# Kernel tuning notes

Measured on AMD Instinct MI355X. Metric: run time of the kernel, lower is better.

Reference implementation:

```python
import jax, jax.numpy as jnp
import numpy as np

B, T, E, L = 512, 20, 256, 2          # batch, path_length, embedding_size, LSTM layers
VE, VA = 50000, 1000                  # entity / action vocab
M = 4                                 # use_entity_embeddings -> m=4
D = M * E                             # LSTMCell input size  (1024)
H = M * 256                           # LSTMCell hidden size (m*hidden_size = 1024)


def setup_inputs() -> dict:
    key = jax.random.key(0)
    ks = jax.random.split(key, 14)
    s = 1.0 / np.sqrt(H)
    ent_emb = (jax.random.normal(ks[0], (VE, 2 * E), jnp.float32) * 0.02).at[0].set(0.0)
    rel_emb = (jax.random.normal(ks[1], (VA, 2 * E), jnp.float32) * 0.02).at[0].set(0.0)
    inp = {
        "entity_batch": jax.random.randint(ks[2], (B, T), 1, VE, jnp.int32),
        "relation_batch": jax.random.randint(ks[3], (B, T), 1, VA, jnp.int32),
        "query_relations": jax.random.randint(ks[4], (B,), 1, VA, jnp.int32),
        "data_length": jax.random.randint(ks[5], (B,), 1, T + 1, jnp.int32),
        "ent_emb": ent_emb,
        "rel_emb": rel_emb,
        "W_ih": jax.random.uniform(ks[6], (L, 4 * H, D), jnp.float32, -s, s),
        "W_hh": jax.random.uniform(ks[7], (L, 4 * H, H), jnp.float32, -s, s),
        "b_ih": jax.random.uniform(ks[8], (L, 4 * H), jnp.float32, -s, s),
        "b_hh": jax.random.uniform(ks[9], (L, 4 * H), jnp.float32, -s, s),
        "W1": jax.random.uniform(ks[10], (4 * 256, H), jnp.float32, -s, s),   # Linear(m*hidden, 4*hidden)
        "b1": jax.random.uniform(ks[11], (4 * 256,), jnp.float32, -s, s),
        "W2": jax.random.uniform(ks[12], (2, 4 * 256), jnp.float32, -0.05, 0.05),
        "b2": jax.random.uniform(ks[13], (2,), jnp.float32, -0.05, 0.05),
    }
    return inp


def reference(entity_batch, relation_batch, query_relations, data_length,
              ent_emb, rel_emb, W_ih, W_hh, b_ih, b_hh, W1, b1, W2, b2):
    # action encoder: concat(relation_emb, entity_emb) -> [B, T, 4E]
    x = jnp.concatenate([rel_emb[relation_batch], ent_emb[entity_batch]], axis=-1)
    xs = jnp.swapaxes(x, 0, 1)  # [T, B, 4E]

    def step(carry, xt):
        hs, cs = carry  # each [L, B, H]
        new_h, new_c = [], []
        for i in range(L):
            # NOTE: faithful to source — every layer consumes xt (prev_action_embeddings)
            g = xt @ W_ih[i].T + b_ih[i] + hs[i] @ W_hh[i].T + b_hh[i]  # [B, 4H]
            gi, gf, gg, go = jnp.split(g, 4, axis=-1)
            c = jax.nn.sigmoid(gf) * cs[i] + jax.nn.sigmoid(gi) * jnp.tanh(gg)
            h = jax.nn.sigmoid(go) * jnp.tanh(c)
            new_h.append(h)
            new_c.append(c)
        return (jnp.stack(new_h), jnp.stack(new_c)), new_h[-1]

    init = (jnp.zeros((L, B, H), jnp.float32), jnp.zeros((L, B, H), jnp.float32))
    _, outs = jax.lax.scan(step, init, xs)       # [T, B, H]
    outs = jnp.swapaxes(outs, 0, 1)              # [B, T, H]

    # gather output at position data_length-1 per row
    idx = (data_length - 1).astype(jnp.int32)[:, None, None]
    sel = jnp.take_along_axis(outs, idx, axis=1)[:, 0, :]  # [B, H]

    # policy MLP: Linear -> ReLU -> Linear -> ReLU, then squeeze (no-op for [B,2])
    y = jax.nn.relu(sel @ W1.T + b1)
    y = jax.nn.relu(y @ W2.T + b2)
    return jnp.squeeze(y)
```

## Files before the change

### kernel.cpp

```cpp
#include <hip/hip_runtime.h>

typedef __bf16 bf16x8 __attribute__((ext_vector_type(8)));
typedef __bf16 bf16x4 __attribute__((ext_vector_type(4)));
typedef float  f32x4  __attribute__((ext_vector_type(4)));

#define MFMA16 __builtin_amdgcn_mfma_f32_16x16x32_bf16

__device__ __forceinline__ float fsig(float x)  { return 1.f / (1.f + __expf(-x)); }
__device__ __forceinline__ float ftanh(float x) { return 1.f - 2.f / (__expf(2.f * x) + 1.f); }


__global__ __launch_bounds__(512) void prep(
    const float* __restrict__ Wih, const float* __restrict__ Whh,
    const float* __restrict__ W1,  const float* __restrict__ bih,
    const float* __restrict__ bhh, const int* __restrict__ dlen,
    __bf16* __restrict__ Wih1, __bf16* __restrict__ Whh1,
    __bf16* __restrict__ W1b,  float* __restrict__ bsum,
    int* __restrict__ perm, int* __restrict__ dl_s, int* __restrict__ n_act)
{
    const int tid = threadIdx.x;
    if (blockIdx.x < 2048) {
        const size_t L1 = 4096UL * 1024UL;
        size_t i = (size_t)blockIdx.x * 512 + tid;
        float4 a = *(const float4*)(Wih + L1 + i * 4);
        float4 b = *(const float4*)(Whh + L1 + i * 4);
        bf16x4 av = { (__bf16)a.x, (__bf16)a.y, (__bf16)a.z, (__bf16)a.w };
        bf16x4 bv = { (__bf16)b.x, (__bf16)b.y, (__bf16)b.z, (__bf16)b.w };
        *(bf16x4*)(Wih1 + i * 4) = av;
        *(bf16x4*)(Whh1 + i * 4) = bv;
        W1b[i] = (__bf16)W1[i];
        if (i < 4096) bsum[i] = bih[4096 + i] + bhh[4096 + i];
    } else {
        __shared__ int sdl[512];
        const int b = tid;
        const int dl = dlen[b];
        sdl[b] = dl;
        __syncthreads();
        int pos = 0;
        for (int j = 0; j < 512; ++j) {
            const int dj = sdl[j];
            pos += (dj > dl) || (dj == dl && j < b);
        }
        perm[pos] = b;
        dl_s[pos] = dl;
        if (b < 20) {
            int cnt = 0;
            for (int j = 0; j < 512; ++j) cnt += (sdl[j] > b);
            n_act[b] = cnt;
        }
    }
}

__global__ __launch_bounds__(256) void gather_x(
    const int* __restrict__ ent, const int* __restrict__ rel,
    const float* __restrict__ ent_emb, const float* __restrict__ rel_emb,
    const int* __restrict__ perm, __bf16* __restrict__ xbf)
{
    int bid = blockIdx.x;
    int sb = bid / 20, t = bid - sb * 20;
    int bo = perm[sb];
    int tid = threadIdx.x;
    int col = (tid & 127) * 4;
    const float* src = (tid < 128)
        ? (rel_emb + (size_t)rel[bo * 20 + t] * 512 + col)
        : (ent_emb + (size_t)ent[bo * 20 + t] * 512 + col);
    float4 v = *(const float4*)src;
    bf16x4 o = { (__bf16)v.x, (__bf16)v.y, (__bf16)v.z, (__bf16)v.w };
    int outcol = (tid < 128) ? col : (512 + col);
    *(bf16x4*)(xbf + (size_t)(t * 512 + sb) * 1024 + outcol) = o;
}

template<bool RELU, bool SKIP>
__global__ __launch_bounds__(256) void gemm_bias(
    const __bf16* __restrict__ A, const __bf16* __restrict__ B,
    const float* __restrict__ bias, __bf16* __restrict__ C,
    int M, int N, int K, const int* __restrict__ nact)
{
    const int m0 = blockIdx.y * 128, n0 = blockIdx.x * 128;
    if (SKIP) {
        if ((m0 & 511) >= nact[m0 >> 9]) return;
    }
    __shared__ __bf16 As[2][128 * 64];
    __shared__ __bf16 Bs[2][128 * 64];
    const int tid = threadIdx.x;
    const int w = tid >> 6, lane = tid & 63;
    const int wr = (w >> 1) * 64, wc = (w & 1) * 64;
    const int srow = w * 32 + (lane >> 3);
    const int scol = (((lane & 7) ^ (lane >> 3)) << 3);
    const int wofs = srow * 64 + (lane & 7) * 8;

    f32x4 acc[4][4] = {};
    bf16x8 ar[4], br[4];

#pragma unroll
    for (int j = 0; j < 4; ++j) {
        ar[j] = *(const bf16x8*)(A + (size_t)(m0 + srow + j * 8) * K + scol);
        br[j] = *(const bf16x8*)(B + (size_t)(n0 + srow + j * 8) * K + scol);
    }
    for (int k0 = 0, i = 0; k0 < K; k0 += 64, ++i) {
        const int cur = i & 1;
#pragma unroll
        for (int j = 0; j < 4; ++j) {
            *(bf16x8*)&As[cur][wofs + j * 512] = ar[j];
            *(bf16x8*)&Bs[cur][wofs + j * 512] = br[j];
        }
        if (k0 + 64 < K) {
#pragma unroll
            for (int j = 0; j < 4; ++j) {
                ar[j] = *(const bf16x8*)(A + (size_t)(m0 + srow + j * 8) * K + k0 + 64 + scol);
                br[j] = *(const bf16x8*)(B + (size_t)(n0 + srow + j * 8) * K + k0 + 64 + scol);
            }
        }
        __syncthreads();
#pragma unroll
        for (int ks = 0; ks < 2; ++ks) {
            const int ko = (((ks * 4 + (lane >> 4)) ^ (lane & 7)) << 3);
            bf16x8 af[4], bb[4];
#pragma unroll
            for (int ii = 0; ii < 4; ++ii)
                af[ii] = *(const bf16x8*)&As[cur][(wr + ii * 16 + (lane & 15)) * 64 + ko];
#pragma unroll
            for (int j = 0; j < 4; ++j)
                bb[j] = *(const bf16x8*)&Bs[cur][(wc + j * 16 + (lane & 15)) * 64 + ko];
#pragma unroll
            for (int ii = 0; ii < 4; ++ii)
#pragma unroll
                for (int j = 0; j < 4; ++j)
                    acc[ii][j] = MFMA16(af[ii], bb[j], acc[ii][j], 0, 0, 0);
        }
    }
    const int rbase = m0 + wr + (lane >> 4) * 4;
    const int cbase = n0 + wc + (lane & 15);
#pragma unroll
    for (int j = 0; j < 4; ++j) {
        const int col = cbase + j * 16;
        const float bv = bias[col];
#pragma unroll
        for (int i = 0; i < 4; ++i)
#pragma unroll
            for (int r = 0; r < 4; ++r) {
                float v = acc[i][j][r] + bv;
                if (RELU) v = fmaxf(v, 0.f);
                C[(size_t)(rbase + i * 16 + r) * N + col] = (__bf16)v;
            }
    }
}

__global__ __launch_bounds__(256) void lstm_step(
    const __bf16* __restrict__ h_in, const __bf16* __restrict__ Whh,
    const __bf16* __restrict__ Xg, float* __restrict__ cst,
    __bf16* __restrict__ h_out, __bf16* __restrict__ sel,
    const int* __restrict__ dl_s, const int* __restrict__ perm,
    const int* __restrict__ n_act, int t)
{
    const int nt = n_act[t];
    const int m0 = blockIdx.y * 32;
    if (m0 >= nt) return;
    __shared__ __bf16 As[2][32 * 64];
    __shared__ __bf16 Bs[2][128 * 64];
    const int tid = threadIdx.x;
    const int w = tid >> 6, lane = tid & 63;
    const int j0 = blockIdx.x * 32;
    const int rh  = w >> 1;
    const int chq = w & 1;

    const int brow = tid >> 3;
    const int seg  = tid & 7;
    const int swc  = ((seg ^ (brow & 7)) << 3);
    const __bf16* gB = Whh + (size_t)(j0 + brow) * 1024 + swc;
    const __bf16* gA = h_in + (size_t)(m0 + brow) * 1024 + swc;

    f32x4 a0 = {0,0,0,0}, a1 = {0,0,0,0}, a2 = {0,0,0,0}, a3 = {0,0,0,0};
    bf16x8 rb0, rb1, rb2, rb3, ra;

    rb0 = *(const bf16x8*)(gB);
    rb1 = *(const bf16x8*)(gB + 1024UL * 1024);
    rb2 = *(const bf16x8*)(gB + 2048UL * 1024);
    rb3 = *(const bf16x8*)(gB + 3072UL * 1024);
    ra  = *(const bf16x8*)(gA);

    for (int k0 = 0, i = 0; k0 < 1024; k0 += 64, ++i) {
        const int cur = i & 1;
        *(bf16x8*)&Bs[cur][(0 * 32 + brow) * 64 + seg * 8] = rb0;
        *(bf16x8*)&Bs[cur][(1 * 32 + brow) * 64 + seg * 8] = rb1;
        *(bf16x8*)&Bs[cur][(2 * 32 + brow) * 64 + seg * 8] = rb2;
        *(bf16x8*)&Bs[cur][(3 * 32 + brow) * 64 + seg * 8] = rb3;
        *(bf16x8*)&As[cur][brow * 64 + seg * 8] = ra;
        if (k0 + 64 < 1024) {
            rb0 = *(const bf16x8*)(gB + k0 + 64);
            rb1 = *(const bf16x8*)(gB + 1024UL * 1024 + k0 + 64);
            rb2 = *(const bf16x8*)(gB + 2048UL * 1024 + k0 + 64);
            rb3 = *(const bf16x8*)(gB + 3072UL * 1024 + k0 + 64);
            ra  = *(const bf16x8*)(gA + k0 + 64);
        }
        __syncthreads();
#pragma unroll
        for (int ks = 0; ks < 2; ++ks) {
            const int ko = (((ks * 4 + (lane >> 4)) ^ (lane & 7)) << 3);
            bf16x8 av = *(const bf16x8*)&As[cur][(rh * 16 + (lane & 15)) * 64 + ko];
            bf16x8 b0 = *(const bf16x8*)&Bs[cur][(0 * 32 + chq * 16 + (lane & 15)) * 64 + ko];
            bf16x8 b1 = *(const bf16x8*)&Bs[cur][(1 * 32 + chq * 16 + (lane & 15)) * 64 + ko];
            bf16x8 b2 = *(const bf16x8*)&Bs[cur][(2 * 32 + chq * 16 + (lane & 15)) * 64 + ko];
            bf16x8 b3 = *(const bf16x8*)&Bs[cur][(3 * 32 + chq * 16 + (lane & 15)) * 64 + ko];
            a0 = MFMA16(av, b0, a0, 0, 0, 0);
            a1 = MFMA16(av, b1, a1, 0, 0, 0);
            a2 = MFMA16(av, b2, a2, 0, 0, 0);
            a3 = MFMA16(av, b3, a3, 0, 0, 0);
        }
    }
    const int ch  = j0 + chq * 16 + (lane & 15);
    const int rb_ = m0 + rh * 16 + (lane >> 4) * 4;
#pragma unroll
    for (int r = 0; r < 4; ++r) {
        const int b = rb_ + r;
        if (b >= nt) continue;
        const __bf16* xg = Xg + (size_t)(t * 512 + b) * 4096 + ch;
        float gi = a0[r] + (float)xg[0];
        float gf = a1[r] + (float)xg[1024];
        float gg = a2[r] + (float)xg[2048];
        float go = a3[r] + (float)xg[3072];
        const size_t ix = (size_t)b * 1024 + ch;
        float cn = fsig(gf) * cst[ix] + fsig(gi) * ftanh(gg);
        cst[ix] = cn;
        float hv = fsig(go) * ftanh(cn);
        h_out[ix] = (__bf16)hv;
        if (dl_s[b] == t + 1)
            sel[(size_t)perm[b] * 1024 + ch] = (__bf16)hv;
    }
}

__global__ __launch_bounds__(256) void mlp2(
    const __bf16* __restrict__ y1, const float* __restrict__ W2,
    const float* __restrict__ b2, float* __restrict__ out)
{
    int b = blockIdx.x, tid = threadIdx.x;
    float s0 = 0.f, s1 = 0.f;
    for (int k = tid; k < 1024; k += 256) {
        float v = (float)y1[(size_t)b * 1024 + k];
        s0 += v * W2[k];
        s1 += v * W2[1024 + k];
    }
#pragma unroll
    for (int o = 32; o > 0; o >>= 1) {
        s0 += __shfl_down(s0, o);
        s1 += __shfl_down(s1, o);
    }
    __shared__ float red[8];
    if ((tid & 63) == 0) { red[(tid >> 6) * 2] = s0; red[(tid >> 6) * 2 + 1] = s1; }
    __syncthreads();
    if (tid == 0) {
        float a0 = red[0] + red[2] + red[4] + red[6] + b2[0];
        float a1 = red[1] + red[3] + red[5] + red[7] + b2[1];
        out[b * 2 + 0] = fmaxf(a0, 0.f);
        out[b * 2 + 1] = fmaxf(a1, 0.f);
    }
}

extern "C" void kernel_launch(void* const* d_in, const int* in_sizes, int n_in,
                              void* d_out, int out_size, void* d_ws, size_t ws_size,
                              hipStream_t stream) {
    const int*   ent     = (const int*)d_in[0];
    const int*   rel     = (const int*)d_in[1];
    const int*   dlen    = (const int*)d_in[3];
    const float* ent_emb = (const float*)d_in[4];
    const float* rel_emb = (const float*)d_in[5];
    const float* Wih     = (const float*)d_in[6];
    const float* Whh     = (const float*)d_in[7];
    const float* bih     = (const float*)d_in[8];
    const float* bhh     = (const float*)d_in[9];
    const float* W1      = (const float*)d_in[10];
    const float* b1      = (const float*)d_in[11];
    const float* W2      = (const float*)d_in[12];
    const float* b2      = (const float*)d_in[13];
    float* out = (float*)d_out;

    char* ws = (char*)d_ws;
    size_t off = 0;
    auto alloc = [&](size_t bytes) -> void* {
        void* p = ws + off; off += (bytes + 255) & ~(size_t)255; return p;
    };
    __bf16* xbf   = (__bf16*)alloc(10240UL * 1024 * 2);
    __bf16* Wih1  = (__bf16*)alloc(4096UL * 1024 * 2);
    __bf16* Whh1  = (__bf16*)alloc(4096UL * 1024 * 2);
    __bf16* W1b   = (__bf16*)alloc(1024UL * 1024 * 2);
    float*  bsum  = (float*) alloc(4096UL * 4);
    __bf16* Xg    = (__bf16*)alloc(10240UL * 4096 * 2);
    __bf16* hA    = (__bf16*)alloc(512UL * 1024 * 2);
    __bf16* hB    = (__bf16*)alloc(512UL * 1024 * 2);
    float*  cst   = (float*) alloc(512UL * 1024 * 4);
    __bf16* selb  = (__bf16*)alloc(512UL * 1024 * 2);
    __bf16* y1b   = (__bf16*)alloc(512UL * 1024 * 2);
    int*    permb = (int*)   alloc(512 * 4);
    int*    dl_s  = (int*)   alloc(512 * 4);
    int*    n_act = (int*)   alloc(32 * 4);

    prep<<<dim3(2049), dim3(512), 0, stream>>>(
        Wih, Whh, W1, bih, bhh, dlen,
        Wih1, Whh1, W1b, bsum, permb, dl_s, n_act);
    gather_x<<<dim3(10240), dim3(256), 0, stream>>>(
        ent, rel, ent_emb, rel_emb, permb, xbf);
    gemm_bias<false, true><<<dim3(32, 80), dim3(256), 0, stream>>>(
        xbf, Wih1, bsum, Xg, 10240, 4096, 1024, n_act);

    hipMemsetAsync(hA, 0, 512UL * 1024 * 2, stream);
    hipMemsetAsync(hB, 0, 512UL * 1024 * 2, stream);
    hipMemsetAsync(cst, 0, 512UL * 1024 * 4, stream);

    for (int t = 0; t < 20; ++t) {
        const __bf16* hi = (t & 1) ? hB : hA;
        __bf16*       ho = (t & 1) ? hA : hB;
        lstm_step<<<dim3(32, 16), dim3(256), 0, stream>>>(
            hi, Whh1, Xg, cst, ho, selb, dl_s, permb, n_act, t);
    }

    gemm_bias<true, false><<<dim3(8, 4), dim3(256), 0, stream>>>(
        selb, W1b, b1, y1b, 512, 1024, 1024, nullptr);
    mlp2<<<dim3(512), dim3(256), 0, stream>>>(y1b, W2, b2, out);
}
```

Baseline: 359.3 us.

## Widen GEMM tile to 128x256 with 8 waves and fold memsets into prep

The bias GEMM now uses 512-thread blocks, each computing a 128x256 output tile with eight waves in a 2x4 arrangement. The global-to-LDS load pattern is reorganized to match, and a second barrier is added per k-step. This raises reuse of A tiles and halves the block count, at the cost of more LDS per block and an extra sync. The three hipMemsetAsync calls are replaced by extra prep blocks that zero the hidden and cell state buffers, removing separate launches.

```diff
diff --git a/kernel.cpp b/kernel.cpp
--- a/kernel.cpp
+++ b/kernel.cpp
@@ -16,7 +16,8 @@
     const float* __restrict__ bhh, const int* __restrict__ dlen,
     __bf16* __restrict__ Wih1, __bf16* __restrict__ Whh1,
     __bf16* __restrict__ W1b,  float* __restrict__ bsum,
-    int* __restrict__ perm, int* __restrict__ dl_s, int* __restrict__ n_act)
+    int* __restrict__ perm, int* __restrict__ dl_s, int* __restrict__ n_act,
+    float4* __restrict__ hA4, float4* __restrict__ hB4, float4* __restrict__ cst4)
 {
     const int tid = threadIdx.x;
     if (blockIdx.x < 2048) {
@@ -30,7 +31,7 @@
         *(bf16x4*)(Whh1 + i * 4) = bv;
         W1b[i] = (__bf16)W1[i];
         if (i < 4096) bsum[i] = bih[4096 + i] + bhh[4096 + i];
-    } else {
+    } else if (blockIdx.x == 2048) {
         __shared__ int sdl[512];
         const int b = tid;
         const int dl = dlen[b];
@@ -48,6 +49,13 @@
             for (int j = 0; j < 512; ++j) cnt += (sdl[j] > b);
             n_act[b] = cnt;
         }
+    } else {
+        const int idx = (blockIdx.x - 2049) * 512 + tid;
+        const float4 z = {0.f, 0.f, 0.f, 0.f};
+        hA4[idx] = z;
+        hB4[idx] = z;
+        cst4[idx] = z;
+        cst4[131072 + idx] = z;
     }
 }
 
@@ -71,45 +79,50 @@
 }
 
 template<bool RELU, bool SKIP>
-__global__ __launch_bounds__(256) void gemm_bias(
+__global__ __launch_bounds__(512, 2) void gemm_bias(
     const __bf16* __restrict__ A, const __bf16* __restrict__ B,
     const float* __restrict__ bias, __bf16* __restrict__ C,
     int M, int N, int K, const int* __restrict__ nact)
 {
-    const int m0 = blockIdx.y * 128, n0 = blockIdx.x * 128;
+    const int m0 = blockIdx.y * 128, n0 = blockIdx.x * 256;
     if (SKIP) {
         if ((m0 & 511) >= nact[m0 >> 9]) return;
     }
     __shared__ __bf16 As[2][128 * 64];
-    __shared__ __bf16 Bs[2][128 * 64];
+    __shared__ __bf16 Bs[2][256 * 64];
     const int tid = threadIdx.x;
     const int w = tid >> 6, lane = tid & 63;
-    const int wr = (w >> 1) * 64, wc = (w & 1) * 64;
-    const int srow = w * 32 + (lane >> 3);
-    const int scol = (((lane & 7) ^ (lane >> 3)) << 3);
-    const int wofs = srow * 64 + (lane & 7) * 8;
+    const int wr = (w >> 2) * 64;
+    const int wc = (w & 3) * 64;
+    const int srow = tid >> 3;
+    const int scol = (((tid & 7) ^ (srow & 7)) << 3);
+    const int wofs = srow * 64 + (tid & 7) * 8;
 
     f32x4 acc[4][4] = {};
-    bf16x8 ar[4], br[4];
-
-#pragma unroll
-    for (int j = 0; j < 4; ++j) {
-        ar[j] = *(const bf16x8*)(A + (size_t)(m0 + srow + j * 8) * K + scol);
-        br[j] = *(const bf16x8*)(B + (size_t)(n0 + srow + j * 8) * K + scol);
-    }
+    bf16x8 ar[2], br[4];
+
+#pragma unroll
+    for (int j = 0; j < 2; ++j)
+        ar[j] = *(const bf16x8*)(A + (size_t)(m0 + j * 64 + srow) * K + scol);
+#pragma unroll
+    for (int j = 0; j < 4; ++j)
+        br[j] = *(const bf16x8*)(B + (size_t)(n0 + j * 64 + srow) * K + scol);
+
     for (int k0 = 0, i = 0; k0 < K; k0 += 64, ++i) {
         const int cur = i & 1;
 #pragma unroll
-        for (int j = 0; j < 4; ++j) {
-            *(bf16x8*)&As[cur][wofs + j * 512] = ar[j];
-            *(bf16x8*)&Bs[cur][wofs + j * 512] = br[j];
-        }
+        for (int j = 0; j < 2; ++j)
+            *(bf16x8*)&As[cur][wofs + j * 4096] = ar[j];
+#pragma unroll
+        for (int j = 0; j < 4; ++j)
+            *(bf16x8*)&Bs[cur][wofs + j * 4096] = br[j];
         if (k0 + 64 < K) {
 #pragma unroll
-            for (int j = 0; j < 4; ++j) {
-                ar[j] = *(const bf16x8*)(A + (size_t)(m0 + srow + j * 8) * K + k0 + 64 + scol);
-                br[j] = *(const bf16x8*)(B + (size_t)(n0 + srow + j * 8) * K + k0 + 64 + scol);
-            }
+            for (int j = 0; j < 2; ++j)
+                ar[j] = *(const bf16x8*)(A + (size_t)(m0 + j * 64 + srow) * K + k0 + 64 + scol);
+#pragma unroll
+            for (int j = 0; j < 4; ++j)
+                br[j] = *(const bf16x8*)(B + (size_t)(n0 + j * 64 + srow) * K + k0 + 64 + scol);
         }
         __syncthreads();
 #pragma unroll
@@ -128,6 +141,7 @@
                 for (int j = 0; j < 4; ++j)
                     acc[ii][j] = MFMA16(af[ii], bb[j], acc[ii][j], 0, 0, 0);
         }
+        __syncthreads();
     }
     const int rbase = m0 + wr + (lane >> 4) * 4;
     const int cbase = n0 + wc + (lane & 15);
@@ -294,17 +308,14 @@
     int*    dl_s  = (int*)   alloc(512 * 4);
     int*    n_act = (int*)   alloc(32 * 4);
 
-    prep<<<dim3(2049), dim3(512), 0, stream>>>(
+    prep<<<dim3(2305), dim3(512), 0, stream>>>(
         Wih, Whh, W1, bih, bhh, dlen,
-        Wih1, Whh1, W1b, bsum, permb, dl_s, n_act);
+        Wih1, Whh1, W1b, bsum, permb, dl_s, n_act,
+        (float4*)hA, (float4*)hB, (float4*)cst);
     gather_x<<<dim3(10240), dim3(256), 0, stream>>>(
         ent, rel, ent_emb, rel_emb, permb, xbf);
-    gemm_bias<false, true><<<dim3(32, 80), dim3(256), 0, stream>>>(
+    gemm_bias<false, true><<<dim3(16, 80), dim3(512), 0, stream>>>(
         xbf, Wih1, bsum, Xg, 10240, 4096, 1024, n_act);
-
-    hipMemsetAsync(hA, 0, 512UL * 1024 * 2, stream);
-    hipMemsetAsync(hB, 0, 512UL * 1024 * 2, stream);
-    hipMemsetAsync(cst, 0, 512UL * 1024 * 4, stream);
 
     for (int t = 0; t < 20; ++t) {
         const __bf16* hi = (t & 1) ? hB : hA;
@@ -313,7 +324,7 @@
             hi, Whh1, Xg, cst, ho, selb, dl_s, permb, n_act, t);
     }
 
-    gemm_bias<true, false><<<dim3(8, 4), dim3(256), 0, stream>>>(
+    gemm_bias<true, false><<<dim3(4, 4), dim3(512), 0, stream>>>(
         selb, W1b, b1, y1b, 512, 1024, 1024, nullptr);
     mlp2<<<dim3(512), dim3(256), 0, stream>>>(y1b, W2, b2, out);
 }
```

Result: slower. 373.5 us (+4.0%).

## Retile LSTM step to 64 rows by 16 hidden units and fold zero-init into prep

Applied to the files above, without the earlier changes.

The recurrent step kernel now tiles 64 batch rows against 16 hidden channels per block (all four gates), instead of 32 rows against 32 channels. This halves the Whh slice each block loads and doubles the A tile, which changes the reuse balance and the grid shape (64x8). The three hipMemsetAsync calls that zeroed h and c state are replaced by extra blocks in the prep kernel, removing separate launches. Coarser row tiles can waste work when few rows stay active at late timesteps.

```diff
diff --git a/kernel.cpp b/kernel.cpp
--- a/kernel.cpp
+++ b/kernel.cpp
@@ -16,7 +16,8 @@
     const float* __restrict__ bhh, const int* __restrict__ dlen,
     __bf16* __restrict__ Wih1, __bf16* __restrict__ Whh1,
     __bf16* __restrict__ W1b,  float* __restrict__ bsum,
-    int* __restrict__ perm, int* __restrict__ dl_s, int* __restrict__ n_act)
+    int* __restrict__ perm, int* __restrict__ dl_s, int* __restrict__ n_act,
+    float4* __restrict__ hA4, float4* __restrict__ hB4, float4* __restrict__ cst4)
 {
     const int tid = threadIdx.x;
     if (blockIdx.x < 2048) {
@@ -30,7 +31,7 @@
         *(bf16x4*)(Whh1 + i * 4) = bv;
         W1b[i] = (__bf16)W1[i];
         if (i < 4096) bsum[i] = bih[4096 + i] + bhh[4096 + i];
-    } else {
+    } else if (blockIdx.x == 2048) {
         __shared__ int sdl[512];
         const int b = tid;
         const int dl = dlen[b];
@@ -48,6 +49,13 @@
             for (int j = 0; j < 512; ++j) cnt += (sdl[j] > b);
             n_act[b] = cnt;
         }
+    } else {
+        const int idx = (blockIdx.x - 2049) * 512 + tid;
+        const float4 z = {0.f, 0.f, 0.f, 0.f};
+        hA4[idx] = z;
+        hB4[idx] = z;
+        cst4[idx] = z;
+        cst4[131072 + idx] = z;
     }
 }
 
@@ -154,62 +162,58 @@
     const int* __restrict__ n_act, int t)
 {
     const int nt = n_act[t];
-    const int m0 = blockIdx.y * 32;
+    const int m0 = blockIdx.y * 64;
     if (m0 >= nt) return;
-    __shared__ __bf16 As[2][32 * 64];
-    __shared__ __bf16 Bs[2][128 * 64];
+    __shared__ __bf16 As[2][64 * 64];
+    __shared__ __bf16 Bs[2][64 * 64];
     const int tid = threadIdx.x;
     const int w = tid >> 6, lane = tid & 63;
-    const int j0 = blockIdx.x * 32;
-    const int rh  = w >> 1;
-    const int chq = w & 1;
-
-    const int brow = tid >> 3;
-    const int seg  = tid & 7;
-    const int swc  = ((seg ^ (brow & 7)) << 3);
-    const __bf16* gB = Whh + (size_t)(j0 + brow) * 1024 + swc;
-    const __bf16* gA = h_in + (size_t)(m0 + brow) * 1024 + swc;
+    const int ch0 = blockIdx.x * 16;
+
+    const int r_  = tid >> 2;
+    const int s0_ = tid & 3, s1_ = s0_ + 4;
+    const int g0 = ((s0_ ^ (r_ & 7)) << 3);
+    const int g1 = ((s1_ ^ (r_ & 7)) << 3);
+    const __bf16* gBr = Whh + (size_t)((r_ >> 4) * 1024 + ch0 + (r_ & 15)) * 1024;
+    const __bf16* gAr = h_in + (size_t)(m0 + r_) * 1024;
 
     f32x4 a0 = {0,0,0,0}, a1 = {0,0,0,0}, a2 = {0,0,0,0}, a3 = {0,0,0,0};
-    bf16x8 rb0, rb1, rb2, rb3, ra;
-
-    rb0 = *(const bf16x8*)(gB);
-    rb1 = *(const bf16x8*)(gB + 1024UL * 1024);
-    rb2 = *(const bf16x8*)(gB + 2048UL * 1024);
-    rb3 = *(const bf16x8*)(gB + 3072UL * 1024);
-    ra  = *(const bf16x8*)(gA);
+    bf16x8 rb0, rb1, ra0, ra1;
+
+    rb0 = *(const bf16x8*)(gBr + g0);
+    rb1 = *(const bf16x8*)(gBr + g1);
+    ra0 = *(const bf16x8*)(gAr + g0);
+    ra1 = *(const bf16x8*)(gAr + g1);
 
     for (int k0 = 0, i = 0; k0 < 1024; k0 += 64, ++i) {
         const int cur = i & 1;
-        *(bf16x8*)&Bs[cur][(0 * 32 + brow) * 64 + seg * 8] = rb0;
-        *(bf16x8*)&Bs[cur][(1 * 32 + brow) * 64 + seg * 8] = rb1;
-        *(bf16x8*)&Bs[cur][(2 * 32 + brow) * 64 + seg * 8] = rb2;
-        *(bf16x8*)&Bs[cur][(3 * 32 + brow) * 64 + seg * 8] = rb3;
-        *(bf16x8*)&As[cur][brow * 64 + seg * 8] = ra;
+        *(bf16x8*)&Bs[cur][r_ * 64 + s0_ * 8] = rb0;
+        *(bf16x8*)&Bs[cur][r_ * 64 + s1_ * 8] = rb1;
+        *(bf16x8*)&As[cur][r_ * 64 + s0_ * 8] = ra0;
+        *(bf16x8*)&As[cur][r_ * 64 + s1_ * 8] = ra1;
         if (k0 + 64 < 1024) {
-            rb0 = *(const bf16x8*)(gB + k0 + 64);
-            rb1 = *(const bf16x8*)(gB + 1024UL * 1024 + k0 + 64);
-            rb2 = *(const bf16x8*)(gB + 2048UL * 1024 + k0 + 64);
-            rb3 = *(const bf16x8*)(gB + 3072UL * 1024 + k0 + 64);
-            ra  = *(const bf16x8*)(gA + k0 + 64);
+            rb0 = *(const bf16x8*)(gBr + g0 + k0 + 64);
+            rb1 = *(const bf16x8*)(gBr + g1 + k0 + 64);
+            ra0 = *(const bf16x8*)(gAr + g0 + k0 + 64);
+            ra1 = *(const bf16x8*)(gAr + g1 + k0 + 64);
         }
         __syncthreads();
 #pragma unroll
         for (int ks = 0; ks < 2; ++ks) {
             const int ko = (((ks * 4 + (lane >> 4)) ^ (lane & 7)) << 3);
-            bf16x8 av = *(const bf16x8*)&As[cur][(rh * 16 + (lane & 15)) * 64 + ko];
-            bf16x8 b0 = *(const bf16x8*)&Bs[cur][(0 * 32 + chq * 16 + (lane & 15)) * 64 + ko];
-            bf16x8 b1 = *(const bf16x8*)&Bs[cur][(1 * 32 + chq * 16 + (lane & 15)) * 64 + ko];
-            bf16x8 b2 = *(const bf16x8*)&Bs[cur][(2 * 32 + chq * 16 + (lane & 15)) * 64 + ko];
-            bf16x8 b3 = *(const bf16x8*)&Bs[cur][(3 * 32 + chq * 16 + (lane & 15)) * 64 + ko];
+            bf16x8 av = *(const bf16x8*)&As[cur][(w * 16 + (lane & 15)) * 64 + ko];
+            bf16x8 b0 = *(const bf16x8*)&Bs[cur][(0 * 16 + (lane & 15)) * 64 + ko];
+            bf16x8 b1 = *(const bf16x8*)&Bs[cur][(1 * 16 + (lane & 15)) * 64 + ko];
+            bf16x8 b2 = *(const bf16x8*)&Bs[cur][(2 * 16 + (lane & 15)) * 64 + ko];
+            bf16x8 b3 = *(const bf16x8*)&Bs[cur][(3 * 16 + (lane & 15)) * 64 + ko];
             a0 = MFMA16(av, b0, a0, 0, 0, 0);
             a1 = MFMA16(av, b1, a1, 0, 0, 0);
             a2 = MFMA16(av, b2, a2, 0, 0, 0);
             a3 = MFMA16(av, b3, a3, 0, 0, 0);
         }
     }
-    const int ch  = j0 + chq * 16 + (lane & 15);
-    const int rb_ = m0 + rh * 16 + (lane >> 4) * 4;
+    const int ch  = ch0 + (lane & 15);
+    const int rb_ = m0 + w * 16 + (lane >> 4) * 4;
 #pragma unroll
     for (int r = 0; r < 4; ++r) {
         const int b = rb_ + r;
@@ -294,22 +298,19 @@
     int*    dl_s  = (int*)   alloc(512 * 4);
     int*    n_act = (int*)   alloc(32 * 4);
 
-    prep<<<dim3(2049), dim3(512), 0, stream>>>(
+    prep<<<dim3(2305), dim3(512), 0, stream>>>(
         Wih, Whh, W1, bih, bhh, dlen,
-        Wih1, Whh1, W1b, bsum, permb, dl_s, n_act);
+        Wih1, Whh1, W1b, bsum, permb, dl_s, n_act,
+        (float4*)hA, (float4*)hB, (float4*)cst);
     gather_x<<<dim3(10240), dim3(256), 0, stream>>>(
         ent, rel, ent_emb, rel_emb, permb, xbf);
     gemm_bias<false, true><<<dim3(32, 80), dim3(256), 0, stream>>>(
         xbf, Wih1, bsum, Xg, 10240, 4096, 1024, n_act);
 
-    hipMemsetAsync(hA, 0, 512UL * 1024 * 2, stream);
-    hipMemsetAsync(hB, 0, 512UL * 1024 * 2, stream);
-    hipMemsetAsync(cst, 0, 512UL * 1024 * 4, stream);
-
     for (int t = 0; t < 20; ++t) {
         const __bf16* hi = (t & 1) ? hB : hA;
         __bf16*       ho = (t & 1) ? hA : hB;
-        lstm_step<<<dim3(32, 16), dim3(256), 0, stream>>>(
+        lstm_step<<<dim3(64, 8), dim3(256), 0, stream>>>(
             hi, Whh1, Xg, cst, ho, selb, dl_s, permb, n_act, t);
     }
 
```

New measurement: 358.1 us. About the same (-0.3%).
